# Kernel tuning notes

Measured on AMD Instinct MI355X. Metric: run time of the kernel, lower is better.

Reference implementation:

```python
import jax, jax.numpy as jnp
import numpy as np
from jax import lax

N = 8192

def _conv(x, w, b):
    # x: NCHW, w: OIHW, valid conv stride 1
    y = lax.conv_general_dilated(x, w, (1, 1), 'VALID',
                                 dimension_numbers=('NCHW', 'OIHW', 'NCHW'))
    return y + b[None, :, None, None]

def _maxpool2(x):
    return lax.reduce_window(x, -jnp.inf, lax.max, (1, 1, 2, 2), (1, 1, 2, 2), 'VALID')

def setup_inputs() -> dict:
    key = jax.random.key(0)
    ks = jax.random.split(key, 13)
    def rn(k, shape, scale):
        return jax.random.normal(k, shape, dtype=jnp.float32) * scale
    inp = {}
    inp['x'] = jax.random.normal(ks[0], (N, 3, 32, 32), dtype=jnp.float32)
    inp['W1'] = rn(ks[1], (6, 3, 5, 5), 0.1)
    inp['b1'] = rn(ks[2], (6,), 0.1)
    inp['W2'] = rn(ks[3], (16, 6, 5, 5), 0.08)
    inp['b2'] = rn(ks[4], (16,), 0.1)
    inp['Wf1'] = rn(ks[5], (120, 400), 0.05)
    inp['bf1'] = rn(ks[6], (120,), 0.05)
    inp['Wf2'] = rn(ks[7], (84, 120), 0.09)
    inp['bf2'] = rn(ks[8], (84,), 0.09)
    inp['Wg'] = rn(ks[9], (10, 84), 0.1)    # GATConv fc weight (no bias)
    inp['attn_l'] = rn(ks[10], (10,), 0.3)  # a_l (src)
    inp['attn_r'] = rn(ks[11], (10,), 0.3)  # a_r (dst)
    inp['bg'] = rn(ks[12], (10,), 0.1)      # GATConv output bias
    return inp

def reference(x, W1, b1, W2, b2, Wf1, bf1, Wf2, bf2, Wg, attn_l, attn_r, bg):
    # CNN feature extractor (LeNet style)
    h = _maxpool2(jax.nn.relu(_conv(x, W1, b1)))   # [N,6,14,14]
    h = _maxpool2(jax.nn.relu(_conv(h, W2, b2)))   # [N,16,5,5]
    h = h.reshape(-1, 16 * 5 * 5)                  # [N,400]
    h = jax.nn.relu(h @ Wf1.T + bf1)               # [N,120]
    h = jax.nn.relu(h @ Wf2.T + bf2)               # [N,84]
    # Single-head GAT over fully-connected graph (incl. self-loops):
    # equivalent dense formulation of DGL GATConv(84,10,1)
    z = h @ Wg.T                                    # [N,10]
    el = z @ attn_l                                 # src scores [N]
    er = z @ attn_r                                 # dst scores [N]
    # e[i,j]: edge src=j -> dst=i
    e = jax.nn.leaky_relu(er[:, None] + el[None, :], negative_slope=0.2)  # [N,N]
    alpha = jax.nn.softmax(e, axis=1)               # softmax over incoming edges
    out = alpha @ z + bg                            # [N,10]
    return out
```

## Files before the change

kernel.cpp:

```cpp
#include <hip/hip_runtime.h>
#include <hip/hip_bf16.h>

typedef _Float16 half8 __attribute__((ext_vector_type(8)));
typedef __attribute__((aligned(8))) half8 half8_a8;
typedef float floatx4 __attribute__((ext_vector_type(4)));

__global__ __launch_bounds__(256) void k_prep(const float* __restrict__ Wf1,
    const float* __restrict__ Wf2, const float* __restrict__ Wg,
    const float* __restrict__ W1, const float* __restrict__ W2,
    _Float16* __restrict__ w1f, _Float16* __restrict__ w2f,
    _Float16* __restrict__ wgf, _Float16* __restrict__ B1,
    _Float16* __restrict__ B2M) {
  const int i = blockIdx.x * 256 + threadIdx.x;
  if (i < 53248) {
    const int n = i / 416, k = i - n * 416;
    w1f[i] = (_Float16)((n < 120 && k < 400) ? Wf1[n * 400 + k] : 0.f);
  } else if (i < 65536) {
    const int j = i - 53248;
    const int n = j >> 7, k = j & 127;
    w2f[j] = (_Float16)((n < 84 && k < 120) ? Wf2[n * 120 + k] : 0.f);
  } else if (i < 67072) {
    const int g = i - 65536;
    const int n = g / 96, k = g - n * 96;
    wgf[g] = (_Float16)((n < 10 && k < 84) ? Wg[n * 84 + k] : 0.f);
  } else if (i < 72192) {
    const int g = i - 67072;
    const int n = g / 160, k = g - n * 160;
    const int co = n >> 2, cy = (n >> 1) & 1, cx = n & 1;
    float v = 0.f;
    if (k < 144 && co < 6) {
      const int ci = k / 48, rj = k - ci * 48, r = rj >> 3, j = rj & 7;
      const int ky = r - cy, kx = j - cx;
      if (ky >= 0 && ky < 5 && kx >= 0 && kx < 5)
        v = W1[((co * 3 + ci) * 5 + ky) * 5 + kx];
    }
    B1[g] = (_Float16)v;
  } else if (i < 76288) {
    const int g = i - 72192;
    const int n = g >> 8, k = g & 255;
    float v = 0.f;
    if (k < 240) {
      const int ci = k / 40, rem = k - ci * 40, r = rem >> 3, j = rem & 7;
      if (j < 5) v = W2[((n * 6 + ci) * 5 + r) * 5 + j];
    }
    B2M[g] = (_Float16)v;
  }
}

__global__ __launch_bounds__(256) void k_conv1(const float* __restrict__ x,
    const _Float16* __restrict__ B1, const float* __restrict__ b1,
    _Float16* __restrict__ h1) {
  __shared__ __align__(16) char sm[31104];
  const int t = threadIdx.x;
  const int n0 = blockIdx.x * 2;
  const float4* x4 = (const float4*)(x + (size_t)n0 * 3072);
  for (int i = t; i < 1536; i += 256) {
    const float4 v = x4[i];
    const int img = i / 768, rem = i - img * 768;
    const int ci = rem >> 8, rem2 = rem & 255;
    const int y = rem2 >> 3, c = rem2 & 7;
    union { _Float16 h[2]; unsigned u; } p01, p23;
    p01.h[0] = (_Float16)v.x; p01.h[1] = (_Float16)v.y;
    p23.h[0] = (_Float16)v.z; p23.h[1] = (_Float16)v.w;
    char* ch = sm + (img * 3 + ci) * 5184 + y * 80;
    *(uint2*)(ch + 8 * c) = make_uint2(p01.u, p23.u);
    *(unsigned*)(ch + 2592 + 8 * c - 4) = p01.u;
    *(unsigned*)(ch + 2592 + 8 * c) = p23.u;
  }
  if (t < 192) {
    const int img = t / 96, r2 = t - img * 96, ci = r2 >> 5, y = r2 & 31;
    *(unsigned*)(sm + (img * 3 + ci) * 5184 + 2592 + y * 80 + 60) = 0u;
  }
  __syncthreads();
  const int w = t >> 6, lane = t & 63;
  const int l16 = lane & 15, q = lane >> 4;
  int C1[5];
#pragma unroll
  for (int kc = 0; kc < 5; kc++) {
    const int pidx = kc * 4 + q;
    C1[kc] = (pidx < 18) ? (pidx / 6) * 5184 + (pidx % 6) * 80 : 0;
  }
  half8 bfr[2][5];
#pragma unroll
  for (int nt = 0; nt < 2; nt++)
#pragma unroll
    for (int kc = 0; kc < 5; kc++)
      bfr[nt][kc] =
          *(const half8*)(B1 + (size_t)(nt * 16 + l16) * 160 + kc * 32 + q * 8);
  const int co0 = l16 >> 2, co1 = 4 + (l16 >> 2);
  const float bias0 = b1[co0 < 6 ? co0 : 0];
  const float bias1 = (co1 < 6) ? b1[co1] : 0.f;
  const bool lact = (l16 & 3) == 0;
  for (int mt = w; mt < 25; mt += 4) {
    const int m = min(mt * 16 + l16, 391);
    const int img = m / 196, p = m - img * 196;
    const int py = p / 14, px = p - py * 14;
    const int colOff = 4 * px + ((px & 1) ? 2588 : 0);
    const char* base = sm + img * 15552 + py * 160 + colOff;
    half8 a[5];
#pragma unroll
    for (int kc = 0; kc < 5; kc++) a[kc] = *(const half8_a8*)(base + C1[kc]);
#pragma unroll
    for (int nt = 0; nt < 2; nt++) {
      floatx4 acc;
#pragma unroll
      for (int r = 0; r < 4; r++) acc[r] = 0.f;
#pragma unroll
      for (int kc = 0; kc < 5; kc++)
        acc = __builtin_amdgcn_mfma_f32_16x16x32_f16(a[kc], bfr[nt][kc], acc, 0, 0, 0);
      const int co = nt ? co1 : co0;
      const float bias = nt ? bias1 : bias0;
      const bool act = lact && co < 6;
#pragma unroll
      for (int r = 0; r < 4; r++) {
        float v = acc[r];
        v = fmaxf(v, __shfl_xor(v, 1, 64));
        v = fmaxf(v, __shfl_xor(v, 2, 64));
        const int mm = mt * 16 + q * 4 + r;
        if (act && mm < 392) {
          const int im = mm / 196, pp = mm - im * 196;
          h1[(size_t)(n0 + im) * 1176 + co * 196 + pp] =
              (_Float16)fmaxf(v + bias, 0.f);
        }
      }
    }
  }
}

__global__ __launch_bounds__(256) void k_conv2(const _Float16* __restrict__ h1,
    const _Float16* __restrict__ B2M, const float* __restrict__ b2,
    _Float16* __restrict__ h2) {
  __shared__ __align__(16) char sm[22272];
  const int t = threadIdx.x;
  const int n0 = blockIdx.x * 2;
  if (t < 168) {
    const int img = t / 84, rem = t - img * 84;
    const int ci = rem / 14, y = rem - ci * 14;
    const unsigned* src =
        (const unsigned*)(h1 + (size_t)(n0 + img) * 1176 + ci * 196 + y * 14);
    unsigned u[10];
#pragma unroll
    for (int k = 0; k < 7; k++) u[k] = src[k];
    u[7] = 0u; u[8] = 0u; u[9] = 0u;
    char* base = sm + img * 11136 + ci * 1856 + y * 32;
#pragma unroll
    for (int ww = 0; ww < 8; ww++) {
      *(unsigned*)(base + 4 * ww) = u[ww];
      *(unsigned*)(base + 464 + 4 * ww) = (u[ww] >> 16) | (u[ww + 1] << 16);
      *(unsigned*)(base + 928 + 4 * ww) = u[ww + 1];
      *(unsigned*)(base + 1392 + 4 * ww) = (u[ww + 1] >> 16) | (u[ww + 2] << 16);
    }
  }
  if (t < 32) {
    const int im = t >> 4;
    h2[(size_t)(n0 + im) * 416 + 400 + (t & 15)] = (_Float16)0.f;
  }
  __syncthreads();
  const int w = t >> 6, lane = t & 63;
  const int l16 = lane & 15, q = lane >> 4;
  int C2[8];
#pragma unroll
  for (int kc = 0; kc < 8; kc++) {
    const int pidx = kc * 4 + q;
    C2[kc] = (pidx < 30) ? (pidx / 5) * 1856 + (pidx % 5) * 32 : 0;
  }
  half8 bfr[8];
#pragma unroll
  for (int kc = 0; kc < 8; kc++)
    bfr[kc] = *(const half8*)(B2M + (size_t)l16 * 256 + kc * 32 + q * 8);
  const float bias = b2[l16];
  for (int mt = w; mt < 13; mt += 4) {
    const int m = min(mt * 16 + l16, 199);
    const int pos = m >> 2, cy = (m >> 1) & 1, cx = m & 1;
    const int img = pos / 25, p = pos - img * 25;
    const int py = p / 5, px = p - py * 5;
    const int h = 2 * px + cx, s = h & 3;
    const char* base =
        sm + img * 11136 + s * 464 + (2 * py + cy) * 32 + (h - s) * 2;
    half8 a[8];
#pragma unroll
    for (int kc = 0; kc < 8; kc++) a[kc] = *(const half8_a8*)(base + C2[kc]);
    floatx4 acc;
#pragma unroll
    for (int r = 0; r < 4; r++) acc[r] = 0.f;
#pragma unroll
    for (int kc = 0; kc < 8; kc++)
      acc = __builtin_amdgcn_mfma_f32_16x16x32_f16(a[kc], bfr[kc], acc, 0, 0, 0);
    const float v = fmaxf(fmaxf(acc[0], acc[1]), fmaxf(acc[2], acc[3]));
    const int posL = mt * 4 + q;
    if (posL < 50) {
      const int im = posL / 25, pp = posL - im * 25;
      h2[(size_t)(n0 + im) * 416 + l16 * 25 + pp] =
          (_Float16)fmaxf(v + bias, 0.f);
    }
  }
}

__global__ __launch_bounds__(256) void k_mlp(
    const _Float16* __restrict__ h2,
    const _Float16* __restrict__ w1,
    const float* __restrict__ bf1,
    const _Float16* __restrict__ w2,
    const float* __restrict__ bf2,
    const _Float16* __restrict__ wg,
    const float* __restrict__ al, const float* __restrict__ ar,
    float* __restrict__ z, float* __restrict__ el, float* __restrict__ er) {
  __shared__ __align__(16) _Float16 h3s[32 * 136];
  __shared__ __align__(16) _Float16 h4s[32 * 104];
  __shared__ float zs[32 * 17];
  const int t = threadIdx.x;
  const int w = t >> 6, lane = t & 63;
  const int l16 = lane & 15, q = lane >> 4;
  const int row0 = blockIdx.x * 32;
  for (int i = t; i < 2176; i += 256) ((float*)h3s)[i] = 0.f;
  for (int i = t; i < 1664; i += 256) ((float*)h4s)[i] = 0.f;
  const int rt = w & 1, cg = w >> 1;
  const int am = row0 + rt * 16 + l16;
  floatx4 acc[4];
#pragma unroll
  for (int ct = 0; ct < 4; ct++)
#pragma unroll
    for (int r = 0; r < 4; r++) acc[ct][r] = 0.f;
  const half8* Ag = (const half8*)(h2 + (size_t)am * 416 + q * 8);
  for (int kc = 0; kc < 13; kc++) {
    half8 a = Ag[kc * 4];
#pragma unroll
    for (int ct = 0; ct < 4; ct++) {
      const int n = cg * 64 + ct * 16 + l16;
      half8 b = *(const half8*)(w1 + (size_t)n * 416 + kc * 32 + q * 8);
      acc[ct] = __builtin_amdgcn_mfma_f32_16x16x32_f16(a, b, acc[ct], 0, 0, 0);
    }
  }
  __syncthreads();
#pragma unroll
  for (int ct = 0; ct < 4; ct++) {
    const int n = cg * 64 + ct * 16 + l16;
    if (n < 120) {
      const float bias = bf1[n];
#pragma unroll
      for (int r = 0; r < 4; r++) {
        const int rr = rt * 16 + q * 4 + r;
        h3s[rr * 136 + n] = (_Float16)fmaxf(acc[ct][r] + bias, 0.f);
      }
    }
  }
  __syncthreads();
  const int cbase2 = (w >> 1) * 3;
  floatx4 acc2[3];
#pragma unroll
  for (int ct = 0; ct < 3; ct++)
#pragma unroll
    for (int r = 0; r < 4; r++) acc2[ct][r] = 0.f;
  const _Float16* A2 = h3s + (rt * 16 + l16) * 136 + q * 8;
  for (int kc = 0; kc < 4; kc++) {
    half8 a = *(const half8*)(A2 + kc * 32);
#pragma unroll
    for (int ct = 0; ct < 3; ct++) {
      const int n = (cbase2 + ct) * 16 + l16;
      half8 b = *(const half8*)(w2 + (size_t)n * 128 + kc * 32 + q * 8);
      acc2[ct] = __builtin_amdgcn_mfma_f32_16x16x32_f16(a, b, acc2[ct], 0, 0, 0);
    }
  }
  __syncthreads();
#pragma unroll
  for (int ct = 0; ct < 3; ct++) {
    const int n = (cbase2 + ct) * 16 + l16;
    if (n < 84) {
      const float bias = bf2[n];
#pragma unroll
      for (int r = 0; r < 4; r++) {
        const int rr = rt * 16 + q * 4 + r;
        h4s[rr * 104 + n] = (_Float16)fmaxf(acc2[ct][r] + bias, 0.f);
      }
    }
  }
  __syncthreads();
  if (w < 2) {
    floatx4 acc3;
#pragma unroll
    for (int r = 0; r < 4; r++) acc3[r] = 0.f;
    const _Float16* A3 = h4s + (w * 16 + l16) * 104 + q * 8;
    for (int kc = 0; kc < 3; kc++) {
      half8 a = *(const half8*)(A3 + kc * 32);
      half8 b = *(const half8*)(wg + (size_t)l16 * 96 + kc * 32 + q * 8);
      acc3 = __builtin_amdgcn_mfma_f32_16x16x32_f16(a, b, acc3, 0, 0, 0);
    }
#pragma unroll
    for (int r = 0; r < 4; r++) {
      const int rr = w * 16 + q * 4 + r;
      zs[rr * 17 + l16] = acc3[r];
      if (l16 < 10) z[(size_t)(row0 + rr) * 10 + l16] = acc3[r];
    }
  }
  __syncthreads();
  if (t < 32) {
    float e1 = 0.f, e2 = 0.f;
#pragma unroll
    for (int d = 0; d < 10; d++) {
      const float zv = zs[t * 17 + d];
      e1 += zv * al[d];
      e2 += zv * ar[d];
    }
    el[row0 + t] = e1;
    er[row0 + t] = e2;
  }
}

__global__ __launch_bounds__(256) void k_elmax(const float* __restrict__ el,
                                               float* __restrict__ out) {
  __shared__ float red[4];
  const int t = threadIdx.x;
  float m = -1e30f;
  for (int i = t; i < 8192; i += 256) m = fmaxf(m, el[i]);
#pragma unroll
  for (int off = 32; off > 0; off >>= 1) m = fmaxf(m, __shfl_down(m, off, 64));
  if ((t & 63) == 0) red[t >> 6] = m;
  __syncthreads();
  if (t == 0) out[0] = fmaxf(fmaxf(red[0], red[1]), fmaxf(red[2], red[3]));
}

__global__ __launch_bounds__(256) void k_attn(const float* __restrict__ z,
    const float* __restrict__ el, const float* __restrict__ er,
    const float* __restrict__ elmax, float* __restrict__ part) {
  __shared__ __align__(16) float zsm[256 * 12];
  const int t = threadIdx.x;
  const int i = blockIdx.x * 256 + t;
  const int split = blockIdx.y;
  const int jbase = split * 256;
  for (int idx = t; idx < 2560; idx += 256) {
    int jj = idx / 10, d = idx - jj * 10;
    zsm[jj * 12 + d] = z[(size_t)jbase * 10 + idx];
  }
  zsm[t * 12 + 10] = el[jbase + t];
  const float eri = er[i];
  const float mx = elmax[0];
  const float s0 = eri + mx;
  const float mi = fmaxf(s0, 0.2f * s0);
  float num[10];
#pragma unroll
  for (int d = 0; d < 10; d++) num[d] = 0.f;
  float den = 0.f;
  __syncthreads();
  for (int jj = 0; jj < 256; jj++) {
    const float4 za = *(const float4*)(zsm + jj * 12);
    const float4 zb = *(const float4*)(zsm + jj * 12 + 4);
    const float2 zc = *(const float2*)(zsm + jj * 12 + 8);
    const float elj = zsm[jj * 12 + 10];
    const float s2 = eri + elj;
    const float lr = fmaxf(s2, 0.2f * s2);
    const float wgt = __expf(lr - mi);
    den += wgt;
    num[0] += wgt * za.x; num[1] += wgt * za.y; num[2] += wgt * za.z; num[3] += wgt * za.w;
    num[4] += wgt * zb.x; num[5] += wgt * zb.y; num[6] += wgt * zb.z; num[7] += wgt * zb.w;
    num[8] += wgt * zc.x; num[9] += wgt * zc.y;
  }
  float* pp = part + (size_t)split * 12 * 8192 + i;
#pragma unroll
  for (int d = 0; d < 10; d++) pp[d * 8192] = num[d];
  pp[10 * 8192] = den;
}

__global__ __launch_bounds__(256) void k_final(const float* __restrict__ part,
    const float* __restrict__ bg, float* __restrict__ out) {
  const int i = blockIdx.x * 256 + threadIdx.x;
  float num[10];
#pragma unroll
  for (int d = 0; d < 10; d++) num[d] = 0.f;
  float den = 0.f;
  for (int s = 0; s < 32; s++) {
    const float* pp = part + (size_t)s * 12 * 8192 + i;
#pragma unroll
    for (int d = 0; d < 10; d++) num[d] += pp[d * 8192];
    den += pp[10 * 8192];
  }
  const float inv = 1.f / den;
#pragma unroll
  for (int d = 0; d < 10; d++) out[(size_t)i * 10 + d] = num[d] * inv + bg[d];
}

extern "C" void kernel_launch(void* const* d_in, const int* in_sizes, int n_in,
                              void* d_out, int out_size, void* d_ws, size_t ws_size,
                              hipStream_t stream) {
  const float* x   = (const float*)d_in[0];
  const float* W1  = (const float*)d_in[1];
  const float* b1  = (const float*)d_in[2];
  const float* W2  = (const float*)d_in[3];
  const float* b2  = (const float*)d_in[4];
  const float* Wf1 = (const float*)d_in[5];
  const float* bf1 = (const float*)d_in[6];
  const float* Wf2 = (const float*)d_in[7];
  const float* bf2 = (const float*)d_in[8];
  const float* Wg  = (const float*)d_in[9];
  const float* al  = (const float*)d_in[10];
  const float* ar  = (const float*)d_in[11];
  const float* bg  = (const float*)d_in[12];
  float* out = (float*)d_out;

  float* ws = (float*)d_ws;
  _Float16* h1f = (_Float16*)ws;
  float* p = ws + (size_t)8192 * 588;
  _Float16* h2f = (_Float16*)p;
  p += (size_t)8192 * 208;
  float* z   = p; p += (size_t)8192 * 10;
  float* el  = p; p += 8192;
  float* er  = p; p += 8192;
  float* emx = p; p += 16;
  _Float16* w1f = (_Float16*)p; p += 26624;
  _Float16* w2f = (_Float16*)p; p += 6144;
  _Float16* wgf = (_Float16*)p; p += 768;
  _Float16* B1g = (_Float16*)p; p += 2560;
  _Float16* B2g = (_Float16*)p; p += 2048;
  float* part = ws;

  k_prep<<<298, 256, 0, stream>>>(Wf1, Wf2, Wg, W1, W2, w1f, w2f, wgf, B1g, B2g);
  k_conv1<<<4096, 256, 0, stream>>>(x, B1g, b1, h1f);
  k_conv2<<<4096, 256, 0, stream>>>(h1f, B2g, b2, h2f);
  k_mlp<<<256, 256, 0, stream>>>(h2f, w1f, bf1, w2f, bf2, wgf, al, ar, z, el, er);
  k_elmax<<<1, 256, 0, stream>>>(el, emx);
  dim3 ag(32, 32);
  k_attn<<<ag, 256, 0, stream>>>(z, el, er, emx, part);
  k_final<<<32, 256, 0, stream>>>(part, bg, out);
}
```

Before: 295.7 us.

## Restructure conv1 with sliding-row MFMA reuse, DPP pooling, and multi-row attention blocking

Conv1 is reorganised so each wave handles one image half and slides a window of A fragments down the rows. It reuses four of six loaded fragments per output row, pads K to 192 with a repacked B1 layout, and replaces the shuffle-based 2x2 max pooling with DPP lane swaps. Stores become packed half2 writes. The attention kernel now has each thread process four destination rows, so one shared-memory z read serves four rows, and the grid shrinks accordingly. k_final is rewritten to spread the 32-way partial reduction across 256 blocks with a shared-memory tree. These changes cut LDS traffic and instruction overhead but raise register pressure in the attention and conv1 kernels.

```diff
diff --git a/kernel.cpp b/kernel.cpp
--- a/kernel.cpp
+++ b/kernel.cpp
@@ -4,6 +4,13 @@
 typedef _Float16 half8 __attribute__((ext_vector_type(8)));
 typedef __attribute__((aligned(8))) half8 half8_a8;
 typedef float floatx4 __attribute__((ext_vector_type(4)));
+
+__device__ __forceinline__ float pool4_dpp(float v) {
+  int s1 = __builtin_amdgcn_update_dpp(0, __float_as_int(v), 0xB1, 0xF, 0xF, true);
+  float v1 = fmaxf(v, __int_as_float(s1));
+  int s2 = __builtin_amdgcn_update_dpp(0, __float_as_int(v1), 0x4E, 0xF, 0xF, true);
+  return fmaxf(v1, __int_as_float(s2));
+}
 
 __global__ __launch_bounds__(256) void k_prep(const float* __restrict__ Wf1,
     const float* __restrict__ Wf2, const float* __restrict__ Wg,
@@ -23,20 +30,21 @@
     const int g = i - 65536;
     const int n = g / 96, k = g - n * 96;
     wgf[g] = (_Float16)((n < 10 && k < 84) ? Wg[n * 84 + k] : 0.f);
-  } else if (i < 72192) {
+  } else if (i < 73216) {
     const int g = i - 67072;
-    const int n = g / 160, k = g - n * 160;
+    const int n = g / 192, k = g - n * 192;
     const int co = n >> 2, cy = (n >> 1) & 1, cx = n & 1;
+    const int pidx = k >> 3, j = k & 7;
+    const int r = pidx >> 2, ci = pidx & 3;
     float v = 0.f;
-    if (k < 144 && co < 6) {
-      const int ci = k / 48, rj = k - ci * 48, r = rj >> 3, j = rj & 7;
+    if (co < 6 && ci < 3) {
       const int ky = r - cy, kx = j - cx;
       if (ky >= 0 && ky < 5 && kx >= 0 && kx < 5)
         v = W1[((co * 3 + ci) * 5 + ky) * 5 + kx];
     }
     B1[g] = (_Float16)v;
-  } else if (i < 76288) {
-    const int g = i - 72192;
+  } else if (i < 77312) {
+    const int g = i - 73216;
     const int n = g >> 8, k = g & 255;
     float v = 0.f;
     if (k < 240) {
@@ -62,66 +70,76 @@
     union { _Float16 h[2]; unsigned u; } p01, p23;
     p01.h[0] = (_Float16)v.x; p01.h[1] = (_Float16)v.y;
     p23.h[0] = (_Float16)v.z; p23.h[1] = (_Float16)v.w;
-    char* ch = sm + (img * 3 + ci) * 5184 + y * 80;
-    *(uint2*)(ch + 8 * c) = make_uint2(p01.u, p23.u);
-    *(unsigned*)(ch + 2592 + 8 * c - 4) = p01.u;
-    *(unsigned*)(ch + 2592 + 8 * c) = p23.u;
+    char* row = sm + (img * 3 + ci) * 5184 + y * 80;
+    *(uint2*)(row + 8 * c) = make_uint2(p01.u, p23.u);
+    *(unsigned*)(row + 2596 + 8 * c) = p01.u;
+    *(unsigned*)(row + 2600 + 8 * c) = p23.u;
   }
   if (t < 192) {
     const int img = t / 96, r2 = t - img * 96, ci = r2 >> 5, y = r2 & 31;
-    *(unsigned*)(sm + (img * 3 + ci) * 5184 + 2592 + y * 80 + 60) = 0u;
-  }
-  __syncthreads();
-  const int w = t >> 6, lane = t & 63;
+    *(unsigned*)(sm + (img * 3 + ci) * 5184 + 2596 + y * 80 + 64) = 0u;
+  }
+  __syncthreads();
+  const int w4 = t >> 6, lane = t & 63;
   const int l16 = lane & 15, q = lane >> 4;
-  int C1[5];
-#pragma unroll
-  for (int kc = 0; kc < 5; kc++) {
-    const int pidx = kc * 4 + q;
-    C1[kc] = (pidx < 18) ? (pidx / 6) * 5184 + (pidx % 6) * 80 : 0;
-  }
-  half8 bfr[2][5];
+  const int px = l16;
+  const int colOff = (px & 1) ? (2596 + 4 * px) : (4 * px);
+  const char* base = sm + ((q == 3) ? 0 : q * 5184) + colOff;
+  half8 bfr[2][6];
 #pragma unroll
   for (int nt = 0; nt < 2; nt++)
 #pragma unroll
-    for (int kc = 0; kc < 5; kc++)
+    for (int kc = 0; kc < 6; kc++)
       bfr[nt][kc] =
-          *(const half8*)(B1 + (size_t)(nt * 16 + l16) * 160 + kc * 32 + q * 8);
-  const int co0 = l16 >> 2, co1 = 4 + (l16 >> 2);
-  const float bias0 = b1[co0 < 6 ? co0 : 0];
+          *(const half8*)(B1 + (size_t)(nt * 16 + l16) * 192 + kc * 32 + q * 8);
+  const int co_n = l16 >> 2;
+  const int co1 = 4 + co_n;
+  const float bias0 = b1[co_n];
   const float bias1 = (co1 < 6) ? b1[co1] : 0.f;
-  const bool lact = (l16 & 3) == 0;
-  for (int mt = w; mt < 25; mt += 4) {
-    const int m = min(mt * 16 + l16, 391);
-    const int img = m / 196, p = m - img * 196;
-    const int py = p / 14, px = p - py * 14;
-    const int colOff = 4 * px + ((px & 1) ? 2588 : 0);
-    const char* base = sm + img * 15552 + py * 160 + colOff;
-    half8 a[5];
-#pragma unroll
-    for (int kc = 0; kc < 5; kc++) a[kc] = *(const half8_a8*)(base + C1[kc]);
-#pragma unroll
-    for (int nt = 0; nt < 2; nt++) {
-      floatx4 acc;
-#pragma unroll
-      for (int r = 0; r < 4; r++) acc[r] = 0.f;
-#pragma unroll
-      for (int kc = 0; kc < 5; kc++)
-        acc = __builtin_amdgcn_mfma_f32_16x16x32_f16(a[kc], bfr[nt][kc], acc, 0, 0, 0);
-      const int co = nt ? co1 : co0;
-      const float bias = nt ? bias1 : bias0;
-      const bool act = lact && co < 6;
-#pragma unroll
-      for (int r = 0; r < 4; r++) {
-        float v = acc[r];
-        v = fmaxf(v, __shfl_xor(v, 1, 64));
-        v = fmaxf(v, __shfl_xor(v, 2, 64));
-        const int mm = mt * 16 + q * 4 + r;
-        if (act && mm < 392) {
-          const int im = mm / 196, pp = mm - im * 196;
-          h1[(size_t)(n0 + im) * 1176 + co * 196 + pp] =
-              (_Float16)fmaxf(v + bias, 0.f);
-        }
+  const int img_w = w4 >> 1, pyh = w4 & 1;
+  const int py0 = pyh * 7;
+  const char* ibase = base + img_w * 15552;
+  half8 a[6];
+#pragma unroll
+  for (int r = 0; r < 6; r++)
+    a[r] = *(const half8_a8*)(ibase + (2 * py0 + r) * 80);
+  const size_t ob = (size_t)(n0 + img_w) * 1176;
+  const bool store_lane = (l16 & 3) == 0;
+  for (int it = 0; it < 7; ++it) {
+    const int py = py0 + it;
+    floatx4 acc0, acc1;
+#pragma unroll
+    for (int r = 0; r < 4; r++) { acc0[r] = 0.f; acc1[r] = 0.f; }
+#pragma unroll
+    for (int kc = 0; kc < 6; kc++) {
+      acc0 = __builtin_amdgcn_mfma_f32_16x16x32_f16(a[kc], bfr[0][kc], acc0, 0, 0, 0);
+      acc1 = __builtin_amdgcn_mfma_f32_16x16x32_f16(a[kc], bfr[1][kc], acc1, 0, 0, 0);
+    }
+    if (it < 6) {
+      a[0] = a[2]; a[1] = a[3]; a[2] = a[4]; a[3] = a[5];
+      a[4] = *(const half8_a8*)(ibase + (2 * py + 6) * 80);
+      a[5] = *(const half8_a8*)(ibase + (2 * py + 7) * 80);
+    }
+    float p0[4], p1[4];
+#pragma unroll
+    for (int r = 0; r < 4; r++) {
+      p0[r] = fmaxf(pool4_dpp(acc0[r]) + bias0, 0.f);
+      p1[r] = fmaxf(pool4_dpp(acc1[r]) + bias1, 0.f);
+    }
+    if (store_lane) {
+      union { _Float16 h[2]; unsigned u; } s01, s23;
+      s01.h[0] = (_Float16)p0[0]; s01.h[1] = (_Float16)p0[1];
+      s23.h[0] = (_Float16)p0[2]; s23.h[1] = (_Float16)p0[3];
+      _Float16* dst = h1 + ob + co_n * 196 + py * 14 + q * 4;
+      *(unsigned*)dst = s01.u;
+      if (q < 3) *(unsigned*)(dst + 2) = s23.u;
+      if (co1 < 6) {
+        union { _Float16 h[2]; unsigned u; } t01, t23;
+        t01.h[0] = (_Float16)p1[0]; t01.h[1] = (_Float16)p1[1];
+        t23.h[0] = (_Float16)p1[2]; t23.h[1] = (_Float16)p1[3];
+        _Float16* dst1 = h1 + ob + co1 * 196 + py * 14 + q * 4;
+        *(unsigned*)dst1 = t01.u;
+        if (q < 3) *(unsigned*)(dst1 + 2) = t23.u;
       }
     }
   }
@@ -197,12 +215,9 @@
 }
 
 __global__ __launch_bounds__(256) void k_mlp(
-    const _Float16* __restrict__ h2,
-    const _Float16* __restrict__ w1,
-    const float* __restrict__ bf1,
-    const _Float16* __restrict__ w2,
-    const float* __restrict__ bf2,
-    const _Float16* __restrict__ wg,
+    const _Float16* __restrict__ h2, const _Float16* __restrict__ w1,
+    const float* __restrict__ bf1, const _Float16* __restrict__ w2,
+    const float* __restrict__ bf2, const _Float16* __restrict__ wg,
     const float* __restrict__ al, const float* __restrict__ ar,
     float* __restrict__ z, float* __restrict__ el, float* __restrict__ er) {
   __shared__ __align__(16) _Float16 h3s[32 * 136];
@@ -324,7 +339,6 @@
     const float* __restrict__ elmax, float* __restrict__ part) {
   __shared__ __align__(16) float zsm[256 * 12];
   const int t = threadIdx.x;
-  const int i = blockIdx.x * 256 + t;
   const int split = blockIdx.y;
   const int jbase = split * 256;
   for (int idx = t; idx < 2560; idx += 256) {
@@ -332,50 +346,79 @@
     zsm[jj * 12 + d] = z[(size_t)jbase * 10 + idx];
   }
   zsm[t * 12 + 10] = el[jbase + t];
-  const float eri = er[i];
+  const int i0 = blockIdx.x * 1024 + t;
   const float mx = elmax[0];
-  const float s0 = eri + mx;
-  const float mi = fmaxf(s0, 0.2f * s0);
-  float num[10];
-#pragma unroll
-  for (int d = 0; d < 10; d++) num[d] = 0.f;
-  float den = 0.f;
-  __syncthreads();
+  float eri[4], mi[4];
+#pragma unroll
+  for (int g = 0; g < 4; g++) {
+    eri[g] = er[i0 + g * 256];
+    const float s0 = eri[g] + mx;
+    mi[g] = fmaxf(s0, 0.2f * s0);
+  }
+  float num[4][10];
+#pragma unroll
+  for (int g = 0; g < 4; g++)
+#pragma unroll
+    for (int d = 0; d < 10; d++) num[g][d] = 0.f;
+  float den[4] = {0.f, 0.f, 0.f, 0.f};
+  __syncthreads();
+#pragma unroll 2
   for (int jj = 0; jj < 256; jj++) {
     const float4 za = *(const float4*)(zsm + jj * 12);
     const float4 zb = *(const float4*)(zsm + jj * 12 + 4);
-    const float2 zc = *(const float2*)(zsm + jj * 12 + 8);
-    const float elj = zsm[jj * 12 + 10];
-    const float s2 = eri + elj;
-    const float lr = fmaxf(s2, 0.2f * s2);
-    const float wgt = __expf(lr - mi);
-    den += wgt;
-    num[0] += wgt * za.x; num[1] += wgt * za.y; num[2] += wgt * za.z; num[3] += wgt * za.w;
-    num[4] += wgt * zb.x; num[5] += wgt * zb.y; num[6] += wgt * zb.z; num[7] += wgt * zb.w;
-    num[8] += wgt * zc.x; num[9] += wgt * zc.y;
-  }
-  float* pp = part + (size_t)split * 12 * 8192 + i;
-#pragma unroll
-  for (int d = 0; d < 10; d++) pp[d * 8192] = num[d];
-  pp[10 * 8192] = den;
+    const float4 zc = *(const float4*)(zsm + jj * 12 + 8);
+    const float elj = zc.z;
+#pragma unroll
+    for (int g = 0; g < 4; g++) {
+      const float s2 = eri[g] + elj;
+      const float lr = fmaxf(s2, 0.2f * s2);
+      const float wgt = __expf(lr - mi[g]);
+      den[g] += wgt;
+      num[g][0] += wgt * za.x; num[g][1] += wgt * za.y;
+      num[g][2] += wgt * za.z; num[g][3] += wgt * za.w;
+      num[g][4] += wgt * zb.x; num[g][5] += wgt * zb.y;
+      num[g][6] += wgt * zb.z; num[g][7] += wgt * zb.w;
+      num[g][8] += wgt * zc.x; num[g][9] += wgt * zc.y;
+    }
+  }
+#pragma unroll
+  for (int g = 0; g < 4; g++) {
+    float* pp = part + (size_t)split * 98304 + i0 + g * 256;
+#pragma unroll
+    for (int d = 0; d < 10; d++) pp[d * 8192] = num[g][d];
+    pp[10 * 8192] = den[g];
+  }
 }
 
 __global__ __launch_bounds__(256) void k_final(const float* __restrict__ part,
     const float* __restrict__ bg, float* __restrict__ out) {
-  const int i = blockIdx.x * 256 + threadIdx.x;
-  float num[10];
-#pragma unroll
-  for (int d = 0; d < 10; d++) num[d] = 0.f;
-  float den = 0.f;
-  for (int s = 0; s < 32; s++) {
-    const float* pp = part + (size_t)s * 12 * 8192 + i;
-#pragma unroll
-    for (int d = 0; d < 10; d++) num[d] += pp[d * 8192];
-    den += pp[10 * 8192];
-  }
-  const float inv = 1.f / den;
-#pragma unroll
-  for (int d = 0; d < 10; d++) out[(size_t)i * 10 + d] = num[d] * inv + bg[d];
+  __shared__ float red[8][32][12];
+  const int t = threadIdx.x;
+  const int i0 = blockIdx.x * 32;
+  const int il = t & 31, sg = t >> 5;
+  float v[11];
+#pragma unroll
+  for (int d = 0; d < 11; d++) v[d] = 0.f;
+  for (int u = 0; u < 4; u++) {
+    const float* pp = part + (size_t)(sg * 4 + u) * 98304 + i0 + il;
+#pragma unroll
+    for (int d = 0; d < 11; d++) v[d] += pp[d * 8192];
+  }
+#pragma unroll
+  for (int d = 0; d < 11; d++) red[sg][il][d] = v[d];
+  __syncthreads();
+  for (int t2 = t; t2 < 352; t2 += 256) {
+    const int ii = t2 / 11, d = t2 - ii * 11;
+    if (d < 10) {
+      float num = 0.f, den = 0.f;
+#pragma unroll
+      for (int s = 0; s < 8; s++) {
+        num += red[s][ii][d];
+        den += red[s][ii][10];
+      }
+      out[(size_t)(i0 + ii) * 10 + d] = num / den + bg[d];
+    }
+  }
 }
 
 extern "C" void kernel_launch(void* const* d_in, const int* in_sizes, int n_in,
@@ -408,16 +451,16 @@
   _Float16* w1f = (_Float16*)p; p += 26624;
   _Float16* w2f = (_Float16*)p; p += 6144;
   _Float16* wgf = (_Float16*)p; p += 768;
-  _Float16* B1g = (_Float16*)p; p += 2560;
+  _Float16* B1g = (_Float16*)p; p += 3072;
   _Float16* B2g = (_Float16*)p; p += 2048;
   float* part = ws;
 
-  k_prep<<<298, 256, 0, stream>>>(Wf1, Wf2, Wg, W1, W2, w1f, w2f, wgf, B1g, B2g);
+  k_prep<<<302, 256, 0, stream>>>(Wf1, Wf2, Wg, W1, W2, w1f, w2f, wgf, B1g, B2g);
   k_conv1<<<4096, 256, 0, stream>>>(x, B1g, b1, h1f);
   k_conv2<<<4096, 256, 0, stream>>>(h1f, B2g, b2, h2f);
   k_mlp<<<256, 256, 0, stream>>>(h2f, w1f, bf1, w2f, bf2, wgf, al, ar, z, el, er);
   k_elmax<<<1, 256, 0, stream>>>(el, emx);
-  dim3 ag(32, 32);
+  dim3 ag(8, 32);
   k_attn<<<ag, 256, 0, stream>>>(z, el, er, emx, part);
-  k_final<<<32, 256, 0, stream>>>(part, bg, out);
-}
+  k_final<<<256, 256, 0, stream>>>(part, bg, out);
+}
```

After: 286.6 us. -3.1%, faster.
